# Optimization experiments

Hardware: AMD Instinct MI355X
Metric: run time of the kernel (lower is better)

The kernel has to match this reference:

```python
import jax, jax.numpy as jnp
import numpy as np

EMBD_DIM = 1024
HEAD_SIZE = 64


def setup_inputs() -> dict:
    key = jax.random.key(0)
    kx, kq, kk, kv = jax.random.split(key, 4)
    x = jax.random.normal(kx, (4, 4096, EMBD_DIM), dtype=jnp.float32)
    # nn.Linear(embd_dim, head_size, bias=False) weights, stored as [C, H] so x @ W
    s = 1.0 / np.sqrt(EMBD_DIM)
    Wq = jax.random.uniform(kq, (EMBD_DIM, HEAD_SIZE), jnp.float32, -s, s)
    Wk = jax.random.uniform(kk, (EMBD_DIM, HEAD_SIZE), jnp.float32, -s, s)
    Wv = jax.random.uniform(kv, (EMBD_DIM, HEAD_SIZE), jnp.float32, -s, s)
    return {"x": x, "Wq": Wq, "Wk": Wk, "Wv": Wv}


def reference(x, Wq, Wk, Wv):
    # q,k,v: [B, T, H]
    q = jnp.einsum("btc,ch->bth", x, Wq)
    k = jnp.einsum("btc,ch->bth", x, Wk)
    v = jnp.einsum("btc,ch->bth", x, Wv)
    scale = k.shape[-1] ** -0.5
    # full [B, T, T] score matrix, as in the original naive implementation
    scores = jnp.einsum("bth,bsh->bts", q, k) * scale
    attn = jax.nn.softmax(scores, axis=-1)
    # dropout p=0.0 -> identity
    out = jnp.einsum("bts,bsh->bth", attn, v)  # [B, T, H]
    return out
```

## Files before the change

### kernel.cpp

```cpp
#include <hip/hip_runtime.h>
#include <hip/hip_bf16.h>

#define B_ 4
#define T_ 4096
#define C_ 1024
#define H_ 64

typedef float  f32x4  __attribute__((ext_vector_type(4)));
typedef short  bf16x8 __attribute__((ext_vector_type(8)));
typedef uint   u32x4  __attribute__((ext_vector_type(4)));

static __device__ __forceinline__ ushort f2bf(float f) {
  union { float f; uint u; } v; v.f = f;
  uint u = v.u;
  u += 0x7FFFu + ((u >> 16) & 1u);
  return (ushort)(u >> 16);
}

static __device__ __forceinline__ uint cvtpk(float s0, float s1) {
  uint r;
  asm("v_cvt_pk_bf16_f32 %0, %1, %2" : "=v"(r) : "v"(s0), "v"(s1));
  return r;
}

static __device__ __forceinline__ void gload_lds16(const void* g, void* l) {
  __builtin_amdgcn_global_load_lds(
      (const __attribute__((address_space(1))) unsigned int*)g,
      (__attribute__((address_space(3))) unsigned int*)l, 16, 0, 0);
}

#define MFMA(a, b, c) __builtin_amdgcn_mfma_f32_16x16x32_bf16(a, b, c, 0, 0, 0)

__global__ __launch_bounds__(256) void wt_prep(const float* __restrict__ Wq,
                                               const float* __restrict__ Wk,
                                               const float* __restrict__ Wv,
                                               ushort* __restrict__ WtF) {
  int idx = blockIdx.x * 256 + threadIdx.x;
  int w = idx >> 16, idx2 = idx & 65535;
  int c = idx2 >> 6, n = idx2 & 63;
  const float* W = (w == 0) ? Wq : (w == 1) ? Wk : Wv;
  float v = W[idx2];
  if (w == 0) v *= 0.18033688011112042f;
  int c64 = c >> 6, kc = (c >> 5) & 1, g = (c >> 3) & 3, j = c & 7;
  int nt = n >> 4, l15 = n & 15;
  size_t dst = ((size_t)((((w * 16 + c64) * 2 + kc) * 4 + nt) * 64 + g * 16 + l15)) * 8 + j;
  WtF[dst] = f2bf(v);
}

__global__ __launch_bounds__(256) void qkv_proj(const float* __restrict__ x,
                                                const ushort* __restrict__ WtF,
                                                ushort* __restrict__ Qg,
                                                char* __restrict__ KaF,
                                                char* __restrict__ VaF) {
  __shared__ __align__(16) ushort wl[2][12288];
  const int tid = threadIdx.x;
  const int lane = tid & 63, wid = tid >> 6;
  const int l15 = lane & 15, g = lane >> 4;
  const int b = blockIdx.x >> 6, rt = blockIdx.x & 63;
  const int wrow = rt * 64 + wid * 16;

  f32x4 acc[3][4];
  #pragma unroll
  for (int w = 0; w < 3; w++)
    #pragma unroll
    for (int nt = 0; nt < 4; nt++) acc[w][nt] = (f32x4)0.0f;

  const float* xr = x + ((size_t)b * T_ + wrow + l15) * C_ + g * 8;

  auto stagew = [&](int buf, int c64) {
    char* dst = (char*)wl[buf] + tid * 16;
    const char* src = (const char*)WtF + (size_t)c64 * 8192 + tid * 16;
    #pragma unroll
    for (int p = 0; p < 6; p++)
      gload_lds16(src + (p >> 1) * 131072 + (p & 1) * 4096, dst + p * 4096);
  };

  f32x4 xp[3][4];
  auto xload = [&](int slot, int t) {
    const float* src = xr + t * 64;
    xp[slot][0] = *(const f32x4*)src;
    xp[slot][1] = *(const f32x4*)(src + 4);
    xp[slot][2] = *(const f32x4*)(src + 32);
    xp[slot][3] = *(const f32x4*)(src + 36);
  };

  stagew(0, 0);
  xload(0, 0);
  xload(1, 1);
  asm volatile("s_waitcnt vmcnt(8)" ::: "memory");
  __builtin_amdgcn_s_barrier();
  __builtin_amdgcn_sched_barrier(0);

  #pragma unroll
  for (int t = 0; t < 16; t++) {
    const int cur = t & 1;
    if (t < 15) stagew(cur ^ 1, t + 1);
    if (t < 14) xload((t + 2) % 3, t + 2);

    const int slot = t % 3;
    bf16x8 xa[2];
    #pragma unroll
    for (int kc = 0; kc < 2; kc++) {
      union { uint u[4]; bf16x8 v; } h;
      f32x4 c0 = xp[slot][2 * kc], c1 = xp[slot][2 * kc + 1];
      h.u[0] = cvtpk(c0[0], c0[1]); h.u[1] = cvtpk(c0[2], c0[3]);
      h.u[2] = cvtpk(c1[0], c1[1]); h.u[3] = cvtpk(c1[2], c1[3]);
      xa[kc] = h.v;
    }
    const char* wb = (const char*)wl[cur] + lane * 16;
    __builtin_amdgcn_s_setprio(1);
    #pragma unroll
    for (int w = 0; w < 3; w++)
      #pragma unroll
      for (int kc = 0; kc < 2; kc++)
        #pragma unroll
        for (int nt = 0; nt < 4; nt++) {
          bf16x8 wf = *(const bf16x8*)(wb + w * 8192 + kc * 4096 + nt * 1024);
          acc[w][nt] = MFMA(xa[kc], wf, acc[w][nt]);
        }
    __builtin_amdgcn_s_setprio(0);

    if (t < 15) {
      if (t < 14) asm volatile("s_waitcnt vmcnt(4)" ::: "memory");
      else        asm volatile("s_waitcnt vmcnt(0)" ::: "memory");
      __builtin_amdgcn_s_barrier();
      __builtin_amdgcn_sched_barrier(0);
    }
  }

  char* kdst = KaF + ((size_t)b * 64 + rt) * 8192;
  char* vdst = VaF + ((size_t)b * 128 + (wrow >> 5)) * 4096;
  #pragma unroll
  for (int nt = 0; nt < 4; nt++) {
    int n = nt * 16 + l15;
    int kc = n >> 5, gp2 = (n >> 3) & 3, j2 = n & 7;
    #pragma unroll
    for (int r = 0; r < 4; r++) {
      int tt = wrow + g * 4 + r;
      Qg[((size_t)b * T_ + tt) * H_ + n] = f2bf(acc[0][nt][r]);
      int key = tt & 63;
      *(ushort*)(kdst + kc * 4096 + (key >> 4) * 1024 +
                 (gp2 * 16 + (key & 15)) * 16 + j2 * 2) = f2bf(acc[1][nt][r]);
      int k5 = tt & 31;
      int gp = ((k5 >> 4) << 1) | ((k5 >> 2) & 1);
      int js = ((k5 >> 3) & 1) * 4 + (k5 & 3);
      *(ushort*)(vdst + nt * 1024 + (gp * 16 + l15) * 16 + js * 2) = f2bf(acc[2][nt][r]);
    }
  }
}

__global__ __launch_bounds__(256) void attn(const ushort* __restrict__ Qg,
                                            const char* __restrict__ KaF,
                                            const char* __restrict__ VaF,
                                            ushort* __restrict__ Op,
                                            float* __restrict__ Ds,
                                            float* __restrict__ out,
                                            int KT) {
  __shared__ __align__(16) char kv[3][16384];
  const int tid = threadIdx.x;
  const int lane = tid & 63, wid = tid >> 6;
  const int bid = blockIdx.x;
  const int b = bid & 3;
  const int qt = (bid >> 2) & 31, s = bid >> 7;
  const int l15 = lane & 15, g = lane >> 4;

  bf16x8 qa[2][2];
  #pragma unroll
  for (int qs = 0; qs < 2; qs++) {
    const ushort* qp = Qg + ((size_t)b * T_ + qt * 128 + wid * 32 + qs * 16 + l15) * H_ + g * 8;
    qa[qs][0] = *(const bf16x8*)qp;
    qa[qs][1] = *(const bf16x8*)(qp + 32);
  }

  union { ushort u[8]; bf16x8 v; } ones_u;
  #pragma unroll
  for (int i = 0; i < 8; i++) ones_u.u[i] = 0x3F80;
  const bf16x8 ones = ones_u.v;

  f32x4 oacc[2][4];
  f32x4 dacc[2];
  #pragma unroll
  for (int qs = 0; qs < 2; qs++) {
    #pragma unroll
    for (int nt = 0; nt < 4; nt++) oacc[qs][nt] = (f32x4)0.0f;
    dacc[qs] = (f32x4)0.0f;
  }

  const char* kbase = KaF + (size_t)b * 64 * 8192;
  const char* vbase = VaF + (size_t)b * 128 * 4096;
  const int it0 = s * KT;

  auto stage = [&](int buf, int it) {
    char* dst = kv[buf] + tid * 16;
    const char* ks = kbase + (size_t)it * 8192 + tid * 16;
    const char* vs = vbase + (size_t)it * 8192 + tid * 16;
    gload_lds16(ks, dst);
    gload_lds16(ks + 4096, dst + 4096);
    gload_lds16(vs, dst + 8192);
    gload_lds16(vs + 4096, dst + 12288);
  };

  stage(0, it0);
  stage(1, it0 + 1);
  asm volatile("s_waitcnt vmcnt(4)" ::: "memory");
  __builtin_amdgcn_s_barrier();
  __builtin_amdgcn_sched_barrier(0);

  int cur = 0;
  for (int it = 0; it < KT; it++) {
    int pfb = cur + 2; if (pfb >= 3) pfb -= 3;
    if (it + 2 < KT) stage(pfb, it0 + it + 2);
    const char* kl = kv[cur];
    const char* vl = kv[cur] + 8192;

    f32x4 sacc[2][4];
    #pragma unroll
    for (int qs = 0; qs < 2; qs++)
      #pragma unroll
      for (int nt = 0; nt < 4; nt++) sacc[qs][nt] = (f32x4)0.0f;
    __builtin_amdgcn_s_setprio(1);
    #pragma unroll
    for (int nt = 0; nt < 4; nt++)
      #pragma unroll
      for (int kc = 0; kc < 2; kc++) {
        bf16x8 ka = *(const bf16x8*)(kl + kc * 4096 + nt * 1024 + lane * 16);
        sacc[0][nt] = MFMA(ka, qa[0][kc], sacc[0][nt]);
        sacc[1][nt] = MFMA(ka, qa[1][kc], sacc[1][nt]);
      }
    __builtin_amdgcn_s_setprio(0);

    #pragma unroll
    for (int kk = 0; kk < 2; kk++) {
      bf16x8 pf2[2];
      #pragma unroll
      for (int qs = 0; qs < 2; qs++) {
        f32x4 sa = sacc[qs][2 * kk], sb = sacc[qs][2 * kk + 1];
        uint x0 = cvtpk(__builtin_amdgcn_exp2f(sa[0]), __builtin_amdgcn_exp2f(sa[1]));
        uint x1 = cvtpk(__builtin_amdgcn_exp2f(sa[2]), __builtin_amdgcn_exp2f(sa[3]));
        uint y0 = cvtpk(__builtin_amdgcn_exp2f(sb[0]), __builtin_amdgcn_exp2f(sb[1]));
        uint y1 = cvtpk(__builtin_amdgcn_exp2f(sb[2]), __builtin_amdgcn_exp2f(sb[3]));
        asm volatile("v_permlane32_swap_b32 %0, %1" : "+v"(x0), "+v"(y0));
        asm volatile("v_permlane32_swap_b32 %0, %1" : "+v"(x1), "+v"(y1));
        union { uint u[4]; bf16x8 v; } pfu;
        pfu.u[0] = x0; pfu.u[1] = x1; pfu.u[2] = y0; pfu.u[3] = y1;
        pf2[qs] = pfu.v;
      }
      __builtin_amdgcn_s_setprio(1);
      #pragma unroll
      for (int ntd = 0; ntd < 4; ntd++) {
        bf16x8 va = *(const bf16x8*)(vl + kk * 4096 + ntd * 1024 + lane * 16);
        oacc[0][ntd] = MFMA(va, pf2[0], oacc[0][ntd]);
        oacc[1][ntd] = MFMA(va, pf2[1], oacc[1][ntd]);
      }
      dacc[0] = MFMA(ones, pf2[0], dacc[0]);
      dacc[1] = MFMA(ones, pf2[1], dacc[1]);
      __builtin_amdgcn_s_setprio(0);
    }

    if (it + 1 < KT) {
      if (it + 2 < KT) asm volatile("s_waitcnt vmcnt(4)" ::: "memory");
      else             asm volatile("s_waitcnt vmcnt(0)" ::: "memory");
      __builtin_amdgcn_s_barrier();
      __builtin_amdgcn_sched_barrier(0);
    }
    cur = cur + 1; if (cur >= 3) cur -= 3;
  }

  #pragma unroll
  for (int qs = 0; qs < 2; qs++) {
    float d = dacc[qs][0];
    const int q = qt * 128 + wid * 32 + qs * 16 + l15;
    if (Op != nullptr) {
      ushort* ob = Op + ((size_t)(s * 4 + b) * T_ + q) * H_;
      #pragma unroll
      for (int nt = 0; nt < 4; nt++) {
        uint2 pk;
        pk.x = cvtpk(oacc[qs][nt][0], oacc[qs][nt][1]);
        pk.y = cvtpk(oacc[qs][nt][2], oacc[qs][nt][3]);
        *(uint2*)(ob + nt * 16 + g * 4) = pk;
      }
      if (g == 0) Ds[(size_t)(s * 4 + b) * T_ + q] = d;
    } else {
      float inv = 1.0f / d;
      float* ob = out + ((size_t)b * T_ + q) * H_;
      #pragma unroll
      for (int nt = 0; nt < 4; nt++)
        #pragma unroll
        for (int r = 0; r < 4; r++) ob[nt * 16 + g * 4 + r] = oacc[qs][nt][r] * inv;
    }
  }
}

__global__ __launch_bounds__(256) void reduce_seg(const ushort* __restrict__ Op,
                                                  const float* __restrict__ Ds,
                                                  float* __restrict__ out, int seg) {
  int i = blockIdx.x * 256 + threadIdx.x;
  size_t e = (size_t)i * 4;
  int row = (int)(e >> 6);
  f32x4 o = (f32x4)0.0f;
  float d = 0.0f;
  for (int s = 0; s < seg; s++) {
    uint2 pk = *(const uint2*)(Op + (size_t)s * ((size_t)B_ * T_ * H_) + e);
    union { uint u; float f; } c0, c1, c2, c3;
    c0.u = (pk.x & 0xFFFFu) << 16; c1.u = (pk.x >> 16) << 16;
    c2.u = (pk.y & 0xFFFFu) << 16; c3.u = (pk.y >> 16) << 16;
    o[0] += c0.f; o[1] += c1.f; o[2] += c2.f; o[3] += c3.f;
    d += Ds[(size_t)s * ((size_t)B_ * T_) + row];
  }
  *(f32x4*)(out + e) = o * (1.0f / d);
}

extern "C" void kernel_launch(void* const* d_in, const int* in_sizes, int n_in,
                              void* d_out, int out_size, void* d_ws, size_t ws_size,
                              hipStream_t stream) {
  const float* x  = (const float*)d_in[0];
  const float* Wq = (const float*)d_in[1];
  const float* Wk = (const float*)d_in[2];
  const float* Wv = (const float*)d_in[3];
  float* out = (float*)d_out;

  char* ws = (char*)d_ws;
  size_t off = 0;
  auto take = [&](size_t n) -> void* {
    void* p = ws + off;
    off = (off + n + 255) & ~(size_t)255;
    return p;
  };
  ushort* Qg  = (ushort*)take((size_t)B_ * T_ * H_ * 2);
  char*   KaF = (char*)take((size_t)B_ * T_ * H_ * 2);
  char*   VaF = (char*)take((size_t)B_ * T_ * H_ * 2);
  ushort* WtF = (ushort*)take((size_t)3 * H_ * C_ * 2);

  int seg = 1;
  ushort* Op = nullptr;
  float* Ds = nullptr;
  for (int sg = 4; sg >= 2; sg >>= 1) {
    size_t need = off + (size_t)sg * B_ * T_ * H_ * 2 + 256 + (size_t)sg * B_ * T_ * 4 + 256;
    if (need <= ws_size) {
      seg = sg;
      Op = (ushort*)take((size_t)sg * B_ * T_ * H_ * 2);
      Ds = (float*)take((size_t)sg * B_ * T_ * 4);
      break;
    }
  }
  int KT = 64 / seg;

  wt_prep<<<768, 256, 0, stream>>>(Wq, Wk, Wv, WtF);
  qkv_proj<<<B_ * 64, 256, 0, stream>>>(x, WtF, Qg, KaF, VaF);
  attn<<<B_ * (T_ / 128) * seg, 256, 0, stream>>>(Qg, KaF, VaF, Op, Ds, out, KT);
  if (Op) reduce_seg<<<(B_ * T_ * H_ / 4 + 255) / 256, 256, 0, stream>>>(Op, Ds, out, seg);
}
```

Measured before the change: 53.74 us.

## Fuse split-KV reduction into attention kernel via last-block atomic counter

Removes the separate reduce_seg launch. Each attention block bumps a per-(batch, query-tile) atomic counter, and the last segment block to finish sums the bf16 partial outputs and denominators for that tile and writes the normalized result. The counters are zeroed in wt_prep. This saves a kernel launch and its tail, at the cost of a serialized reduction done by the last-finishing block and extra fences and atomics.

```diff
diff --git a/kernel.cpp b/kernel.cpp
--- a/kernel.cpp
+++ b/kernel.cpp
@@ -30,11 +30,14 @@
 }
 
 #define MFMA(a, b, c) __builtin_amdgcn_mfma_f32_16x16x32_bf16(a, b, c, 0, 0, 0)
+#define SBAR0() __builtin_amdgcn_sched_barrier(0)
 
 __global__ __launch_bounds__(256) void wt_prep(const float* __restrict__ Wq,
                                                const float* __restrict__ Wk,
                                                const float* __restrict__ Wv,
-                                               ushort* __restrict__ WtF) {
+                                               ushort* __restrict__ WtF,
+                                               int* __restrict__ cnt) {
+  if (blockIdx.x == 0 && threadIdx.x < 128) cnt[threadIdx.x] = 0;
   int idx = blockIdx.x * 256 + threadIdx.x;
   int w = idx >> 16, idx2 = idx & 65535;
   int c = idx2 >> 6, n = idx2 & 63;
@@ -89,7 +92,7 @@
   xload(1, 1);
   asm volatile("s_waitcnt vmcnt(8)" ::: "memory");
   __builtin_amdgcn_s_barrier();
-  __builtin_amdgcn_sched_barrier(0);
+  SBAR0();
 
   #pragma unroll
   for (int t = 0; t < 16; t++) {
@@ -124,7 +127,7 @@
       if (t < 14) asm volatile("s_waitcnt vmcnt(4)" ::: "memory");
       else        asm volatile("s_waitcnt vmcnt(0)" ::: "memory");
       __builtin_amdgcn_s_barrier();
-      __builtin_amdgcn_sched_barrier(0);
+      SBAR0();
     }
   }
 
@@ -155,8 +158,10 @@
                                             ushort* __restrict__ Op,
                                             float* __restrict__ Ds,
                                             float* __restrict__ out,
-                                            int KT) {
+                                            int* __restrict__ cnt,
+                                            int KT, int seg) {
   __shared__ __align__(16) char kv[3][16384];
+  __shared__ int lastFlag;
   const int tid = threadIdx.x;
   const int lane = tid & 63, wid = tid >> 6;
   const int bid = blockIdx.x;
@@ -204,7 +209,7 @@
   stage(1, it0 + 1);
   asm volatile("s_waitcnt vmcnt(4)" ::: "memory");
   __builtin_amdgcn_s_barrier();
-  __builtin_amdgcn_sched_barrier(0);
+  SBAR0();
 
   int cur = 0;
   for (int it = 0; it < KT; it++) {
@@ -261,7 +266,7 @@
       if (it + 2 < KT) asm volatile("s_waitcnt vmcnt(4)" ::: "memory");
       else             asm volatile("s_waitcnt vmcnt(0)" ::: "memory");
       __builtin_amdgcn_s_barrier();
-      __builtin_amdgcn_sched_barrier(0);
+      SBAR0();
     }
     cur = cur + 1; if (cur >= 3) cur -= 3;
   }
@@ -289,25 +294,38 @@
         for (int r = 0; r < 4; r++) ob[nt * 16 + g * 4 + r] = oacc[qs][nt][r] * inv;
     }
   }
-}
-
-__global__ __launch_bounds__(256) void reduce_seg(const ushort* __restrict__ Op,
-                                                  const float* __restrict__ Ds,
-                                                  float* __restrict__ out, int seg) {
-  int i = blockIdx.x * 256 + threadIdx.x;
-  size_t e = (size_t)i * 4;
-  int row = (int)(e >> 6);
-  f32x4 o = (f32x4)0.0f;
-  float d = 0.0f;
-  for (int s = 0; s < seg; s++) {
-    uint2 pk = *(const uint2*)(Op + (size_t)s * ((size_t)B_ * T_ * H_) + e);
-    union { uint u; float f; } c0, c1, c2, c3;
-    c0.u = (pk.x & 0xFFFFu) << 16; c1.u = (pk.x >> 16) << 16;
-    c2.u = (pk.y & 0xFFFFu) << 16; c3.u = (pk.y >> 16) << 16;
-    o[0] += c0.f; o[1] += c1.f; o[2] += c2.f; o[3] += c3.f;
-    d += Ds[(size_t)s * ((size_t)B_ * T_) + row];
-  }
-  *(f32x4*)(out + e) = o * (1.0f / d);
+
+  if (Op != nullptr) {
+    __syncthreads();
+    if (tid == 0) {
+      int old = __hip_atomic_fetch_add(&cnt[bid & 127], 1,
+                                       __ATOMIC_ACQ_REL, __HIP_MEMORY_SCOPE_AGENT);
+      lastFlag = (old == seg - 1);
+    }
+    __syncthreads();
+    if (lastFlag) {
+      __threadfence();
+      const int q0 = qt * 128;
+      #pragma unroll
+      for (int k = 0; k < 8; k++) {
+        int li = k * 256 + tid;
+        int row = q0 + (li >> 4);
+        int h4 = (li & 15) * 4;
+        f32x4 o = (f32x4)0.0f;
+        float d = 0.0f;
+        for (int s2 = 0; s2 < seg; s2++) {
+          const ushort* op = Op + ((size_t)(s2 * 4 + b) * T_ + row) * H_ + h4;
+          uint2 pk = *(const uint2*)op;
+          union { uint u; float f; } c0, c1, c2, c3;
+          c0.u = (pk.x & 0xFFFFu) << 16; c1.u = (pk.x >> 16) << 16;
+          c2.u = (pk.y & 0xFFFFu) << 16; c3.u = (pk.y >> 16) << 16;
+          o[0] += c0.f; o[1] += c1.f; o[2] += c2.f; o[3] += c3.f;
+          d += Ds[(size_t)(s2 * 4 + b) * T_ + row];
+        }
+        *(f32x4*)(out + ((size_t)b * T_ + row) * H_ + h4) = o * (1.0f / d);
+      }
+    }
+  }
 }
 
 extern "C" void kernel_launch(void* const* d_in, const int* in_sizes, int n_in,
@@ -330,6 +348,7 @@
   char*   KaF = (char*)take((size_t)B_ * T_ * H_ * 2);
   char*   VaF = (char*)take((size_t)B_ * T_ * H_ * 2);
   ushort* WtF = (ushort*)take((size_t)3 * H_ * C_ * 2);
+  int*    cnt = (int*)take(128 * sizeof(int));
 
   int seg = 1;
   ushort* Op = nullptr;
@@ -345,8 +364,7 @@
   }
   int KT = 64 / seg;
 
-  wt_prep<<<768, 256, 0, stream>>>(Wq, Wk, Wv, WtF);
+  wt_prep<<<768, 256, 0, stream>>>(Wq, Wk, Wv, WtF, cnt);
   qkv_proj<<<B_ * 64, 256, 0, stream>>>(x, WtF, Qg, KaF, VaF);
-  attn<<<B_ * (T_ / 128) * seg, 256, 0, stream>>>(Qg, KaF, VaF, Op, Ds, out, KT);
-  if (Op) reduce_seg<<<(B_ * T_ * H_ / 4 + 255) / 256, 256, 0, stream>>>(Op, Ds, out, seg);
-}
+  attn<<<B_ * (T_ / 128) * seg, 256, 0, stream>>>(Qg, KaF, VaF, Op, Ds, out, cnt, KT, seg);
+}
```

Measured after the change: 84.86 us. 57.9% more time.
